# Performance work log

Hardware: AMD Instinct MI355X
Metric: run time of the kernel (lower is better)

The kernel has to match this reference:

```python
import jax, jax.numpy as jnp
import numpy as np

N_NODES = 4096
D_MODEL = 1024
MAX_DEPS = 8
N_CLASSES = 64


def setup_inputs() -> dict:
    key = jax.random.key(0)
    k1, k2, k3 = jax.random.split(key, 3)
    questions = jax.random.normal(k1, (N_NODES, D_MODEL), dtype=jnp.float32)
    # Padded dependency lists; every dependency index is strictly < node index,
    # so processing nodes in index order is a valid topological order.
    rng = np.random.default_rng(0)
    dep_idx = np.zeros((N_NODES, MAX_DEPS), dtype=np.int32)
    dep_mask = np.zeros((N_NODES, MAX_DEPS), dtype=np.int32)
    for i in range(1, N_NODES):
        nd = int(rng.integers(1, MAX_DEPS + 1))
        dep_idx[i, :nd] = rng.integers(0, i, size=nd)
        dep_mask[i, :nd] = 1
    W1 = jax.random.normal(k2, (D_MODEL, 2 * D_MODEL), dtype=jnp.float32) * 0.02
    b1 = jnp.zeros((D_MODEL,), dtype=jnp.float32)
    W2 = jax.random.normal(k3, (N_CLASSES, D_MODEL), dtype=jnp.float32) * 0.02
    b2 = jnp.zeros((N_CLASSES,), dtype=jnp.float32)
    return {
        "questions": questions,
        "W1": W1,
        "b1": b1,
        "W2": W2,
        "b2": b2,
        "dep_idx": jnp.asarray(dep_idx),
        "dep_mask": jnp.asarray(dep_mask),
    }


def reference(questions, W1, b1, W2, b2, dep_idx, dep_mask):
    n_nodes, d_model = questions.shape

    def step(answers, xs):
        i, q, deps, mask = xs
        ctx = answers[deps]                       # [MAX_DEPS, d_model] gather
        m = mask.astype(q.dtype)
        # masked mean; all-zero mask -> zero context (matches torch zeros branch)
        ctx_mean = (ctx * m[:, None]).sum(0) / jnp.maximum(m.sum(), 1.0)
        combined = jnp.concatenate([q, ctx_mean])  # [2*d_model]
        h = jax.nn.gelu(combined @ W1.T + b1, approximate=False)
        return answers.at[i].set(h), None

    answers0 = jnp.zeros((n_nodes, d_model), dtype=questions.dtype)
    xs = (jnp.arange(n_nodes), questions, dep_idx, dep_mask)
    answers, _ = jax.lax.scan(step, answers0, xs)
    root_answer = answers[n_nodes - 1]            # root = last node in topo order
    return root_answer @ W2.T + b2                # [n_classes] logits
```

## Files before the change

kernel.cpp:

```cpp
#include <hip/hip_runtime.h>

#define NN 4096
#define DM 1024
#define MD 8
#define NW 256
#define NCOL 4
#define NT 512
#define NWAVE (NT / 64)
#define UR 4
#define MAXL 4097

#define MI_NLEV 0
#define MI_ROOTPOS 1
#define MI_ARRIVE 8
#define MI_LO 1024
#define MI_NL 6144
#define MI_PERM 10240
#define MI_DCNT 14336
#define MI_INV 18432
#define MI_DPOS 22528

typedef __attribute__((ext_vector_type(8))) short bf16x8;
typedef __attribute__((ext_vector_type(8))) unsigned short ushort8;
typedef __attribute__((ext_vector_type(4))) float f32x4;

__device__ __forceinline__ float gelu_f(float x) {
  return 0.5f * x * (1.0f + erff(x * 0.70710678118654752440f));
}
__device__ __forceinline__ unsigned short f2bf(float x) {
  unsigned int u = __builtin_bit_cast(unsigned int, x);
  u += 0x7FFFu + ((u >> 16) & 1u);
  return (unsigned short)(u >> 16);
}
__device__ __forceinline__ float bf2f(unsigned short v) {
  return __builtin_bit_cast(float, (unsigned int)v << 16);
}

__global__ __launch_bounds__(1024) void k_pro(
    const float* __restrict__ Q, const int* __restrict__ dep_idx,
    const int* __restrict__ dep_mask, int* __restrict__ meta,
    unsigned short* __restrict__ Qb) {
  __shared__ unsigned short deps[NN][MD];
  __shared__ unsigned short lvl[NN];
  __shared__ unsigned short liv[NN];
  __shared__ int cnt[2 * NN];
  __shared__ int pos[NN];
  __shared__ int s_max;
  const int t = threadIdx.x;

  if (blockIdx.x != 0) {
    const size_t total = (size_t)NN * DM / 8;
    for (size_t c = (size_t)(blockIdx.x - 1) * 1024 + t; c < total; c += 256 * 1024) {
      const size_t i = c * 8;
      float4 a = *(const float4*)&Q[i];
      float4 b = *(const float4*)&Q[i + 4];
      ushort8 o;
      o[0] = f2bf(a.x); o[1] = f2bf(a.y); o[2] = f2bf(a.z); o[3] = f2bf(a.w);
      o[4] = f2bf(b.x); o[5] = f2bf(b.y); o[6] = f2bf(b.z); o[7] = f2bf(b.w);
      *(ushort8*)&Qb[i] = o;
    }
    return;
  }

  for (int i = t; i < NN; i += 1024) {
    const int4 d0 = *(const int4*)&dep_idx[i * MD];
    const int4 d1 = *(const int4*)&dep_idx[i * MD + 4];
    const int4 m0 = *(const int4*)&dep_mask[i * MD];
    const int4 m1 = *(const int4*)&dep_mask[i * MD + 4];
    deps[i][0] = m0.x ? (unsigned short)(d0.x + 1) : 0;
    deps[i][1] = m0.y ? (unsigned short)(d0.y + 1) : 0;
    deps[i][2] = m0.z ? (unsigned short)(d0.z + 1) : 0;
    deps[i][3] = m0.w ? (unsigned short)(d0.w + 1) : 0;
    deps[i][4] = m1.x ? (unsigned short)(d1.x + 1) : 0;
    deps[i][5] = m1.y ? (unsigned short)(d1.y + 1) : 0;
    deps[i][6] = m1.z ? (unsigned short)(d1.z + 1) : 0;
    deps[i][7] = m1.w ? (unsigned short)(d1.w + 1) : 0;
    lvl[i] = 0;
    liv[i] = (i == NN - 1) ? 1 : 0;
  }
  for (int i = t; i < 2 * NN; i += 1024) cnt[i] = 0;
  if (t == 0) s_max = 0;
  __syncthreads();

  if (t < 64) {
    for (int grp = 0; grp < 64; ++grp) {
      const int i = grp * 64 + t;
      const ushort8 dr = *(const ushort8*)&deps[i][0];
      int lvprev = -1;
      for (;;) {
        int m = 0;
        #pragma unroll
        for (int k = 0; k < MD; ++k) {
          const int dd = dr[k];
          if (dd) { const int l2 = (int)lvl[dd - 1] + 1; m = m > l2 ? m : l2; }
        }
        const bool ch = (m != lvprev);
        lvprev = m;
        lvl[i] = (unsigned short)m;
        if (!__any(ch)) break;
      }
    }
    for (int grp = 63; grp >= 0; --grp) {
      const int i = grp * 64 + t;
      const ushort8 dr = *(const ushort8*)&deps[i][0];
      for (;;) {
        bool ch = false;
        if (liv[i]) {
          #pragma unroll
          for (int k = 0; k < MD; ++k) {
            const int dd = dr[k];
            if (dd && !liv[dd - 1]) { liv[dd - 1] = 1; ch = true; }
          }
        }
        if (!__any(ch)) break;
      }
    }
  }
  __syncthreads();

  for (int i = t; i < NN; i += 1024) {
    const int lv = lvl[i];
    atomicAdd(&cnt[2 * lv + (liv[i] ? 0 : 1)], 1);
    atomicMax(&s_max, lv);
  }
  __syncthreads();
  const int nL = s_max + 1;
  if (t == 0) {
    int off = 0;
    for (int l = 0; l < nL; ++l) {
      meta[MI_LO + l] = off;
      meta[MI_NL + l] = cnt[2 * l];
      const int a = cnt[2 * l], b = cnt[2 * l + 1];
      cnt[2 * l] = off; off += a;
      cnt[2 * l + 1] = off; off += b;
    }
    meta[MI_LO + nL] = off;
    meta[MI_NLEV] = nL;
  }
  __syncthreads();
  for (int i = t; i < NN; i += 1024)
    pos[i] = atomicAdd(&cnt[2 * lvl[i] + (liv[i] ? 0 : 1)], 1);
  __syncthreads();
  for (int i = t; i < NN; i += 1024) {
    const int r = pos[i];
    meta[MI_PERM + r] = i;
    int nd = 0;
    #pragma unroll
    for (int k = 0; k < MD; ++k) {
      const int dd = deps[i][k];
      if (dd) { meta[MI_DPOS + r * MD + nd] = pos[dd - 1]; ++nd; }
    }
    for (int k = nd; k < MD; ++k) meta[MI_DPOS + r * MD + k] = 0;
    meta[MI_DCNT + r] = nd;
    ((float*)meta)[MI_INV + r] = nd ? 1.0f / (float)nd : 0.0f;
  }
  if (t == 0) meta[MI_ROOTPOS] = pos[NN - 1];
  for (int i = t; i < NW; i += 1024) meta[MI_ARRIVE + i] = 0;
}

__global__ __launch_bounds__(256) void k_preq(
    const unsigned short* __restrict__ Qb, const float* __restrict__ W1,
    const float* __restrict__ b1, float* __restrict__ preQ) {
  const int t = threadIdx.x;
  const int wave = t >> 6, lane = t & 63;
  const int wm = wave >> 1, wn = wave & 1;
  const int m0 = blockIdx.y * 128 + wm * 64;
  const int n0 = blockIdx.x * 128 + wn * 64;
  const int lrow = lane & 15;
  const int klo = (lane >> 4) * 8;
  f32x4 acc[4][4] = {};
  for (int k0 = 0; k0 < DM; k0 += 32) {
    bf16x8 af[4];
    #pragma unroll
    for (int f = 0; f < 4; ++f)
      af[f] = *(const bf16x8*)&Qb[(size_t)(m0 + f * 16 + lrow) * DM + k0 + klo];
    bf16x8 bfr[4];
    #pragma unroll
    for (int g = 0; g < 4; ++g) {
      const float* wsrc = &W1[(size_t)(n0 + g * 16 + lrow) * 2048 + k0 + klo];
      float4 w0 = *(const float4*)&wsrc[0];
      float4 w1 = *(const float4*)&wsrc[4];
      bf16x8 bb;
      bb[0] = (short)f2bf(w0.x); bb[1] = (short)f2bf(w0.y);
      bb[2] = (short)f2bf(w0.z); bb[3] = (short)f2bf(w0.w);
      bb[4] = (short)f2bf(w1.x); bb[5] = (short)f2bf(w1.y);
      bb[6] = (short)f2bf(w1.z); bb[7] = (short)f2bf(w1.w);
      bfr[g] = bb;
    }
    #pragma unroll
    for (int f = 0; f < 4; ++f)
      #pragma unroll
      for (int g = 0; g < 4; ++g)
        acc[f][g] = __builtin_amdgcn_mfma_f32_16x16x32_bf16(af[f], bfr[g], acc[f][g], 0, 0, 0);
  }
  float b1v[4];
  #pragma unroll
  for (int g = 0; g < 4; ++g) b1v[g] = b1[n0 + g * 16 + lrow];
  const int mrow = (lane >> 4) * 4;
  #pragma unroll
  for (int f = 0; f < 4; ++f)
    #pragma unroll
    for (int g = 0; g < 4; ++g) {
      const int n = n0 + g * 16 + lrow;
      #pragma unroll
      for (int r = 0; r < 4; ++r)
        preQ[(size_t)(m0 + f * 16 + mrow + r) * DM + n] = acc[f][g][r] + b1v[g];
    }
}

__global__ __launch_bounds__(NT) void k_levels(
    const float* __restrict__ W1, const float* __restrict__ preQ,
    unsigned short* __restrict__ hPb, float4* __restrict__ gPan, int* __restrict__ meta,
    const float* __restrict__ W2, const float* __restrict__ b2, float* __restrict__ out) {
  const int tid = threadIdx.x;
  const int wb = blockIdx.x;
  const int c0 = wb * NCOL;
  const int wave = tid >> 6, lane = tid & 63;
  const int nL = meta[MI_NLEV];
  const int rootRow = meta[MI_ROOTPOS];
  __shared__ int s_lo[MAXL];
  __shared__ int s_nl[MAXL];
  __shared__ float4 preLDS[NT];
  for (int i = tid; i <= nL; i += NT) s_lo[i] = meta[MI_LO + i];
  for (int i = tid; i < nL; i += NT) s_nl[i] = meta[MI_NL + i];
  float4 wreg[NCOL][4];
  #pragma unroll
  for (int cc = 0; cc < NCOL; ++cc)
    #pragma unroll
    for (int q = 0; q < 4; ++q)
      wreg[cc][q] = *(const float4*)&W1[(size_t)(c0 + cc) * 2048 + 1024 + lane * 16 + q * 4];
  __syncthreads();
  float4* gp = gPan + (size_t)wb * NN;
  const float* invA = (const float*)&meta[MI_INV];

  for (int l = 0; l < nL; ++l) {
    const int lo = s_lo[l];
    const int nA = s_nl[l];

    for (int r = lo + tid; r < lo + nA; r += NT) {
      const int node = meta[MI_PERM + r];
      const int nd = meta[MI_DCNT + r];
      const float iv = invA[r];
      const int4 p0 = *(const int4*)&meta[MI_DPOS + r * MD];
      const int4 p1 = *(const int4*)&meta[MI_DPOS + r * MD + 4];
      const int dps[8] = {p0.x, p0.y, p0.z, p0.w, p1.x, p1.y, p1.z, p1.w};
      float sx = 0.f, sy = 0.f, sz = 0.f, sw = 0.f;
      #pragma unroll
      for (int d = 0; d < MD; ++d) {
        float4 v = gp[dps[d]];
        sx += (d < nd) ? v.x : 0.f;
        sy += (d < nd) ? v.y : 0.f;
        sz += (d < nd) ? v.z : 0.f;
        sw += (d < nd) ? v.w : 0.f;
      }
      const float4 pq = (l > 0 && r == lo + tid) ? preLDS[tid]
                                                 : *(const float4*)&preQ[(size_t)node * DM + c0];
      const unsigned short h0 = f2bf(gelu_f(pq.x + sx * iv));
      const unsigned short h1 = f2bf(gelu_f(pq.y + sy * iv));
      const unsigned short h2 = f2bf(gelu_f(pq.z + sz * iv));
      const unsigned short h3 = f2bf(gelu_f(pq.w + sw * iv));
      const unsigned long long u = (unsigned long long)h0 | ((unsigned long long)h1 << 16)
                                 | ((unsigned long long)h2 << 32) | ((unsigned long long)h3 << 48);
      __hip_atomic_store((unsigned long long*)&hPb[(size_t)r * DM + c0], u,
                         __ATOMIC_RELAXED, __HIP_MEMORY_SCOPE_AGENT);
    }
    __syncthreads();
    if (tid == 0)
      __hip_atomic_store(&meta[MI_ARRIVE + wb], l + 1, __ATOMIC_RELAXED, __HIP_MEMORY_SCOPE_AGENT);
    if (l + 1 < nL && tid < s_nl[l + 1]) {
      const int node2 = meta[MI_PERM + s_lo[l + 1] + tid];
      preLDS[tid] = *(const float4*)&preQ[(size_t)node2 * DM + c0];
    }
    if (tid < 64) {
      for (;;) {
        int m = 1 << 30;
        #pragma unroll
        for (int u = 0; u < 4; ++u) {
          int v = __hip_atomic_load(&meta[MI_ARRIVE + tid * 4 + u], __ATOMIC_RELAXED, __HIP_MEMORY_SCOPE_AGENT);
          m = v < m ? v : m;
        }
        #pragma unroll
        for (int off = 1; off < 64; off <<= 1) {
          int o = __shfl_xor(m, off);
          m = o < m ? o : m;
        }
        if (m >= l + 1) break;
        __builtin_amdgcn_s_sleep(1);
      }
    }
    __syncthreads();

    for (int base = wave * UR; base < nA; base += NWAVE * UR) {
      const int cnt = nA - base;
      ushort8 hv[UR][2];
      #pragma unroll
      for (int u = 0; u < UR; ++u) {
        const int r = lo + base + ((u < cnt) ? u : 0);
        const ushort8* h8 = (const ushort8*)&hPb[(size_t)r * DM];
        hv[u][0] = h8[lane * 2];
        hv[u][1] = h8[lane * 2 + 1];
      }
      float rr[UR][NCOL];
      #pragma unroll
      for (int u = 0; u < UR; ++u) {
        float hf[16];
        #pragma unroll
        for (int e = 0; e < 8; ++e) { hf[e] = bf2f(hv[u][0][e]); hf[8 + e] = bf2f(hv[u][1][e]); }
        #pragma unroll
        for (int cc = 0; cc < NCOL; ++cc) {
          float a = 0.f;
          #pragma unroll
          for (int q = 0; q < 4; ++q)
            a += hf[q * 4 + 0] * wreg[cc][q].x + hf[q * 4 + 1] * wreg[cc][q].y
               + hf[q * 4 + 2] * wreg[cc][q].z + hf[q * 4 + 3] * wreg[cc][q].w;
          rr[u][cc] = a;
        }
      }
      #pragma unroll
      for (int off = 1; off < 64; off <<= 1)
        #pragma unroll
        for (int u = 0; u < UR; ++u)
          #pragma unroll
          for (int cc = 0; cc < NCOL; ++cc)
            rr[u][cc] += __shfl_xor(rr[u][cc], off);
      if (lane == 0) {
        #pragma unroll
        for (int u = 0; u < UR; ++u)
          if (u < cnt) gp[lo + base + u] = make_float4(rr[u][0], rr[u][1], rr[u][2], rr[u][3]);
      }
    }
    __syncthreads();
  }

  if (wb == 0) {
    float* red = (float*)preLDS;
    const int j = tid >> 3, kc = tid & 7;
    const ushort8* h8 = (const ushort8*)&hPb[(size_t)rootRow * DM];
    const float* wr2 = W2 + (size_t)j * DM;
    float acc = 0.f;
    for (int k = kc * 128; k < kc * 128 + 128; k += 8) {
      ushort8 hv = h8[k >> 3];
      float4 wa = *(const float4*)&wr2[k];
      float4 wb4 = *(const float4*)&wr2[k + 4];
      acc += bf2f(hv[0]) * wa.x + bf2f(hv[1]) * wa.y + bf2f(hv[2]) * wa.z + bf2f(hv[3]) * wa.w
           + bf2f(hv[4]) * wb4.x + bf2f(hv[5]) * wb4.y + bf2f(hv[6]) * wb4.z + bf2f(hv[7]) * wb4.w;
    }
    red[tid] = acc;
    __syncthreads();
    if (kc == 0) {
      float s = 0.f;
      #pragma unroll
      for (int e = 0; e < 8; ++e) s += red[j * 8 + e];
      out[j] = s + b2[j];
    }
  }
}

extern "C" void kernel_launch(void* const* d_in, const int* in_sizes, int n_in,
                              void* d_out, int out_size, void* d_ws, size_t ws_size,
                              hipStream_t stream) {
  const float* Q        = (const float*)d_in[0];
  const float* W1       = (const float*)d_in[1];
  const float* b1       = (const float*)d_in[2];
  const float* W2       = (const float*)d_in[3];
  const float* b2       = (const float*)d_in[4];
  const int*   dep_idx  = (const int*)d_in[5];
  const int*   dep_mask = (const int*)d_in[6];

  char* ws = (char*)d_ws;
  float*          preQ = (float*)ws;
  unsigned short* hPb  = (unsigned short*)(ws + (16ull << 20));
  unsigned short* Qb   = (unsigned short*)(ws + (24ull << 20));
  float4*         gPan = (float4*)(ws + (32ull << 20));
  int*            meta = (int*)(ws + (48ull << 20));
  float*          out  = (float*)d_out;

  k_pro<<<dim3(257), dim3(1024), 0, stream>>>(Q, dep_idx, dep_mask, meta, Qb);
  k_preq<<<dim3(DM / 128, NN / 128), dim3(256), 0, stream>>>(Qb, W1, b1, preQ);
  k_levels<<<dim3(NW), dim3(NT), 0, stream>>>(W1, preQ, hPb, gPan, meta, W2, b2, out);
}
```

Before: 556.4 us.

## Defer non-urgent panel products past the level barrier and parallelize level computation

Live nodes in each level are split into urgent ones, whose result is consumed by the very next level, and deferred ones. Only the urgent rows' context-panel products are computed before the per-level barrier. The deferred rows are computed during the next level, before the spin-wait, so that work overlaps the cross-block synchronization. The prologue also replaces the single-wave level and liveness propagation with a 1024-thread block-synchronous iteration, and drops one conversion block. This adds more metadata and more block barriers in the prologue.

```diff
diff --git a/kernel.cpp b/kernel.cpp
--- a/kernel.cpp
+++ b/kernel.cpp
@@ -15,10 +15,11 @@
 #define MI_ARRIVE 8
 #define MI_LO 1024
 #define MI_NL 6144
-#define MI_PERM 10240
-#define MI_DCNT 14336
-#define MI_INV 18432
-#define MI_DPOS 22528
+#define MI_NU 10240
+#define MI_PERM 14336
+#define MI_DCNT 18432
+#define MI_INV 22528
+#define MI_DPOS 26624
 
 typedef __attribute__((ext_vector_type(8))) short bf16x8;
 typedef __attribute__((ext_vector_type(8))) unsigned short ushort8;
@@ -40,17 +41,17 @@
     const float* __restrict__ Q, const int* __restrict__ dep_idx,
     const int* __restrict__ dep_mask, int* __restrict__ meta,
     unsigned short* __restrict__ Qb) {
-  __shared__ unsigned short deps[NN][MD];
-  __shared__ unsigned short lvl[NN];
-  __shared__ unsigned short liv[NN];
-  __shared__ int cnt[2 * NN];
+  __shared__ int lvl[NN];
+  __shared__ int liv[NN];
+  __shared__ int mcl[NN];
+  __shared__ int cnt[3 * NN];
   __shared__ int pos[NN];
-  __shared__ int s_max;
+  __shared__ int s_changed, s_max;
   const int t = threadIdx.x;
 
   if (blockIdx.x != 0) {
     const size_t total = (size_t)NN * DM / 8;
-    for (size_t c = (size_t)(blockIdx.x - 1) * 1024 + t; c < total; c += 256 * 1024) {
+    for (size_t c = (size_t)(blockIdx.x - 1) * 1024 + t; c < total; c += 255 * 1024) {
       const size_t i = c * 8;
       float4 a = *(const float4*)&Q[i];
       float4 b = *(const float4*)&Q[i + 4];
@@ -63,65 +64,83 @@
   }
 
   for (int i = t; i < NN; i += 1024) {
+    lvl[i] = 0; liv[i] = (i == NN - 1) ? 1 : 0; mcl[i] = 0x7FFFFFFF;
+  }
+  for (int i = t; i < 3 * NN; i += 1024) cnt[i] = 0;
+  if (t == 0) s_max = 0;
+  __syncthreads();
+
+  for (int u = 0; u < 4; ++u) {
+    const int i = u * 1024 + t;
     const int4 d0 = *(const int4*)&dep_idx[i * MD];
     const int4 d1 = *(const int4*)&dep_idx[i * MD + 4];
     const int4 m0 = *(const int4*)&dep_mask[i * MD];
     const int4 m1 = *(const int4*)&dep_mask[i * MD + 4];
-    deps[i][0] = m0.x ? (unsigned short)(d0.x + 1) : 0;
-    deps[i][1] = m0.y ? (unsigned short)(d0.y + 1) : 0;
-    deps[i][2] = m0.z ? (unsigned short)(d0.z + 1) : 0;
-    deps[i][3] = m0.w ? (unsigned short)(d0.w + 1) : 0;
-    deps[i][4] = m1.x ? (unsigned short)(d1.x + 1) : 0;
-    deps[i][5] = m1.y ? (unsigned short)(d1.y + 1) : 0;
-    deps[i][6] = m1.z ? (unsigned short)(d1.z + 1) : 0;
-    deps[i][7] = m1.w ? (unsigned short)(d1.w + 1) : 0;
-    lvl[i] = 0;
-    liv[i] = (i == NN - 1) ? 1 : 0;
-  }
-  for (int i = t; i < 2 * NN; i += 1024) cnt[i] = 0;
-  if (t == 0) s_max = 0;
-  __syncthreads();
-
-  if (t < 64) {
-    for (int grp = 0; grp < 64; ++grp) {
-      const int i = grp * 64 + t;
-      const ushort8 dr = *(const ushort8*)&deps[i][0];
-      int lvprev = -1;
-      for (;;) {
-        int m = 0;
-        #pragma unroll
-        for (int k = 0; k < MD; ++k) {
-          const int dd = dr[k];
-          if (dd) { const int l2 = (int)lvl[dd - 1] + 1; m = m > l2 ? m : l2; }
-        }
-        const bool ch = (m != lvprev);
-        lvprev = m;
-        lvl[i] = (unsigned short)m;
-        if (!__any(ch)) break;
-      }
-    }
-    for (int grp = 63; grp >= 0; --grp) {
-      const int i = grp * 64 + t;
-      const ushort8 dr = *(const ushort8*)&deps[i][0];
-      for (;;) {
-        bool ch = false;
-        if (liv[i]) {
-          #pragma unroll
-          for (int k = 0; k < MD; ++k) {
-            const int dd = dr[k];
-            if (dd && !liv[dd - 1]) { liv[dd - 1] = 1; ch = true; }
-          }
-        }
-        if (!__any(ch)) break;
-      }
-    }
-  }
-  __syncthreads();
-
+    int my = 0;
+    for (;;) {
+      if (t == 0) s_changed = 0;
+      __syncthreads();
+      int m = 0;
+      if (m0.x) { int l = lvl[d0.x] + 1; m = m > l ? m : l; }
+      if (m0.y) { int l = lvl[d0.y] + 1; m = m > l ? m : l; }
+      if (m0.z) { int l = lvl[d0.z] + 1; m = m > l ? m : l; }
+      if (m0.w) { int l = lvl[d0.w] + 1; m = m > l ? m : l; }
+      if (m1.x) { int l = lvl[d1.x] + 1; m = m > l ? m : l; }
+      if (m1.y) { int l = lvl[d1.y] + 1; m = m > l ? m : l; }
+      if (m1.z) { int l = lvl[d1.z] + 1; m = m > l ? m : l; }
+      if (m1.w) { int l = lvl[d1.w] + 1; m = m > l ? m : l; }
+      if (m > my) { my = m; lvl[i] = m; s_changed = 1; }
+      __syncthreads();
+      if (!s_changed) break;
+    }
+  }
+  for (int u = 3; u >= 0; --u) {
+    const int i = u * 1024 + t;
+    const int4 d0 = *(const int4*)&dep_idx[i * MD];
+    const int4 d1 = *(const int4*)&dep_idx[i * MD + 4];
+    const int4 m0 = *(const int4*)&dep_mask[i * MD];
+    const int4 m1 = *(const int4*)&dep_mask[i * MD + 4];
+    for (;;) {
+      if (t == 0) s_changed = 0;
+      __syncthreads();
+      bool ch = false;
+      if (liv[i]) {
+        if (m0.x && !liv[d0.x]) { liv[d0.x] = 1; ch = true; }
+        if (m0.y && !liv[d0.y]) { liv[d0.y] = 1; ch = true; }
+        if (m0.z && !liv[d0.z]) { liv[d0.z] = 1; ch = true; }
+        if (m0.w && !liv[d0.w]) { liv[d0.w] = 1; ch = true; }
+        if (m1.x && !liv[d1.x]) { liv[d1.x] = 1; ch = true; }
+        if (m1.y && !liv[d1.y]) { liv[d1.y] = 1; ch = true; }
+        if (m1.z && !liv[d1.z]) { liv[d1.z] = 1; ch = true; }
+        if (m1.w && !liv[d1.w]) { liv[d1.w] = 1; ch = true; }
+      }
+      if (ch) s_changed = 1;
+      __syncthreads();
+      if (!s_changed) break;
+    }
+  }
   for (int i = t; i < NN; i += 1024) {
-    const int lv = lvl[i];
-    atomicAdd(&cnt[2 * lv + (liv[i] ? 0 : 1)], 1);
-    atomicMax(&s_max, lv);
+    if (!liv[i]) continue;
+    const int4 d0 = *(const int4*)&dep_idx[i * MD];
+    const int4 d1 = *(const int4*)&dep_idx[i * MD + 4];
+    const int4 m0 = *(const int4*)&dep_mask[i * MD];
+    const int4 m1 = *(const int4*)&dep_mask[i * MD + 4];
+    const int L = lvl[i];
+    if (m0.x) atomicMin(&mcl[d0.x], L);
+    if (m0.y) atomicMin(&mcl[d0.y], L);
+    if (m0.z) atomicMin(&mcl[d0.z], L);
+    if (m0.w) atomicMin(&mcl[d0.w], L);
+    if (m1.x) atomicMin(&mcl[d1.x], L);
+    if (m1.y) atomicMin(&mcl[d1.y], L);
+    if (m1.z) atomicMin(&mcl[d1.z], L);
+    if (m1.w) atomicMin(&mcl[d1.w], L);
+  }
+  __syncthreads();
+  for (int i = t; i < NN; i += 1024) {
+    const int key = liv[i] ? ((mcl[i] == lvl[i] + 1) ? 0 : 1) : 2;
+    mcl[i] = key;
+    atomicAdd(&cnt[3 * lvl[i] + key], 1);
+    atomicMax(&s_max, lvl[i]);
   }
   __syncthreads();
   const int nL = s_max + 1;
@@ -129,27 +148,33 @@
     int off = 0;
     for (int l = 0; l < nL; ++l) {
       meta[MI_LO + l] = off;
-      meta[MI_NL + l] = cnt[2 * l];
-      const int a = cnt[2 * l], b = cnt[2 * l + 1];
-      cnt[2 * l] = off; off += a;
-      cnt[2 * l + 1] = off; off += b;
+      const int a = cnt[3 * l], b = cnt[3 * l + 1], c = cnt[3 * l + 2];
+      meta[MI_NU + l] = a;
+      meta[MI_NL + l] = a + b;
+      cnt[3 * l] = off; off += a;
+      cnt[3 * l + 1] = off; off += b;
+      cnt[3 * l + 2] = off; off += c;
     }
     meta[MI_LO + nL] = off;
     meta[MI_NLEV] = nL;
   }
   __syncthreads();
   for (int i = t; i < NN; i += 1024)
-    pos[i] = atomicAdd(&cnt[2 * lvl[i] + (liv[i] ? 0 : 1)], 1);
+    pos[i] = atomicAdd(&cnt[3 * lvl[i] + mcl[i]], 1);
   __syncthreads();
   for (int i = t; i < NN; i += 1024) {
     const int r = pos[i];
     meta[MI_PERM + r] = i;
+    const int4 d0 = *(const int4*)&dep_idx[i * MD];
+    const int4 d1 = *(const int4*)&dep_idx[i * MD + 4];
+    const int4 m0 = *(const int4*)&dep_mask[i * MD];
+    const int4 m1 = *(const int4*)&dep_mask[i * MD + 4];
+    const int dd[8] = {d0.x, d0.y, d0.z, d0.w, d1.x, d1.y, d1.z, d1.w};
+    const int mm[8] = {m0.x, m0.y, m0.z, m0.w, m1.x, m1.y, m1.z, m1.w};
     int nd = 0;
     #pragma unroll
-    for (int k = 0; k < MD; ++k) {
-      const int dd = deps[i][k];
-      if (dd) { meta[MI_DPOS + r * MD + nd] = pos[dd - 1]; ++nd; }
-    }
+    for (int k = 0; k < MD; ++k)
+      if (mm[k]) { meta[MI_DPOS + r * MD + nd] = pos[dd[k]]; ++nd; }
     for (int k = nd; k < MD; ++k) meta[MI_DPOS + r * MD + k] = 0;
     meta[MI_DCNT + r] = nd;
     ((float*)meta)[MI_INV + r] = nd ? 1.0f / (float)nd : 0.0f;
@@ -220,9 +245,10 @@
   const int rootRow = meta[MI_ROOTPOS];
   __shared__ int s_lo[MAXL];
   __shared__ int s_nl[MAXL];
+  __shared__ int s_nu[MAXL];
   __shared__ float4 preLDS[NT];
   for (int i = tid; i <= nL; i += NT) s_lo[i] = meta[MI_LO + i];
-  for (int i = tid; i < nL; i += NT) s_nl[i] = meta[MI_NL + i];
+  for (int i = tid; i < nL; i += NT) { s_nl[i] = meta[MI_NL + i]; s_nu[i] = meta[MI_NU + i]; }
   float4 wreg[NCOL][4];
   #pragma unroll
   for (int cc = 0; cc < NCOL; ++cc)
@@ -233,11 +259,55 @@
   float4* gp = gPan + (size_t)wb * NN;
   const float* invA = (const float*)&meta[MI_INV];
 
+  auto bphase = [&](int rlo, int rhi) {
+    for (int base = rlo + wave * UR; base < rhi; base += NWAVE * UR) {
+      const int cnt = rhi - base;
+      ushort8 hv[UR][2];
+      #pragma unroll
+      for (int u = 0; u < UR; ++u) {
+        const int r = base + ((u < cnt) ? u : 0);
+        const ushort8* h8 = (const ushort8*)&hPb[(size_t)r * DM];
+        hv[u][0] = h8[lane * 2];
+        hv[u][1] = h8[lane * 2 + 1];
+      }
+      float rr[UR][NCOL];
+      #pragma unroll
+      for (int u = 0; u < UR; ++u) {
+        float hf[16];
+        #pragma unroll
+        for (int e = 0; e < 8; ++e) { hf[e] = bf2f(hv[u][0][e]); hf[8 + e] = bf2f(hv[u][1][e]); }
+        #pragma unroll
+        for (int cc = 0; cc < NCOL; ++cc) {
+          float a = 0.f;
+          #pragma unroll
+          for (int q = 0; q < 4; ++q)
+            a += hf[q * 4 + 0] * wreg[cc][q].x + hf[q * 4 + 1] * wreg[cc][q].y
+               + hf[q * 4 + 2] * wreg[cc][q].z + hf[q * 4 + 3] * wreg[cc][q].w;
+          rr[u][cc] = a;
+        }
+      }
+      #pragma unroll
+      for (int off = 1; off < 64; off <<= 1)
+        #pragma unroll
+        for (int u = 0; u < UR; ++u)
+          #pragma unroll
+          for (int cc = 0; cc < NCOL; ++cc)
+            rr[u][cc] += __shfl_xor(rr[u][cc], off);
+      if (lane == 0) {
+        #pragma unroll
+        for (int u = 0; u < UR; ++u)
+          if (u < cnt) gp[base + u] = make_float4(rr[u][0], rr[u][1], rr[u][2], rr[u][3]);
+      }
+    }
+  };
+
+  int plo = 0, pnu = 0, pnl = 0;
   for (int l = 0; l < nL; ++l) {
     const int lo = s_lo[l];
-    const int nA = s_nl[l];
-
-    for (int r = lo + tid; r < lo + nA; r += NT) {
+    const int nl = s_nl[l];
+    const int nu = s_nu[l];
+
+    for (int r = lo + tid; r < lo + nl; r += NT) {
       const int node = meta[MI_PERM + r];
       const int nd = meta[MI_DCNT + r];
       const float iv = invA[r];
@@ -271,6 +341,7 @@
       const int node2 = meta[MI_PERM + s_lo[l + 1] + tid];
       preLDS[tid] = *(const float4*)&preQ[(size_t)node2 * DM + c0];
     }
+    bphase(plo + pnu, plo + pnl);
     if (tid < 64) {
       for (;;) {
         int m = 1 << 30;
@@ -289,46 +360,8 @@
       }
     }
     __syncthreads();
-
-    for (int base = wave * UR; base < nA; base += NWAVE * UR) {
-      const int cnt = nA - base;
-      ushort8 hv[UR][2];
-      #pragma unroll
-      for (int u = 0; u < UR; ++u) {
-        const int r = lo + base + ((u < cnt) ? u : 0);
-        const ushort8* h8 = (const ushort8*)&hPb[(size_t)r * DM];
-        hv[u][0] = h8[lane * 2];
-        hv[u][1] = h8[lane * 2 + 1];
-      }
-      float rr[UR][NCOL];
-      #pragma unroll
-      for (int u = 0; u < UR; ++u) {
-        float hf[16];
-        #pragma unroll
-        for (int e = 0; e < 8; ++e) { hf[e] = bf2f(hv[u][0][e]); hf[8 + e] = bf2f(hv[u][1][e]); }
-        #pragma unroll
-        for (int cc = 0; cc < NCOL; ++cc) {
-          float a = 0.f;
-          #pragma unroll
-          for (int q = 0; q < 4; ++q)
-            a += hf[q * 4 + 0] * wreg[cc][q].x + hf[q * 4 + 1] * wreg[cc][q].y
-               + hf[q * 4 + 2] * wreg[cc][q].z + hf[q * 4 + 3] * wreg[cc][q].w;
-          rr[u][cc] = a;
-        }
-      }
-      #pragma unroll
-      for (int off = 1; off < 64; off <<= 1)
-        #pragma unroll
-        for (int u = 0; u < UR; ++u)
-          #pragma unroll
-          for (int cc = 0; cc < NCOL; ++cc)
-            rr[u][cc] += __shfl_xor(rr[u][cc], off);
-      if (lane == 0) {
-        #pragma unroll
-        for (int u = 0; u < UR; ++u)
-          if (u < cnt) gp[lo + base + u] = make_float4(rr[u][0], rr[u][1], rr[u][2], rr[u][3]);
-      }
-    }
+    bphase(lo, lo + nu);
+    plo = lo; pnu = nu; pnl = nl;
     __syncthreads();
   }
 
@@ -375,7 +408,7 @@
   int*            meta = (int*)(ws + (48ull << 20));
   float*          out  = (float*)d_out;
 
-  k_pro<<<dim3(257), dim3(1024), 0, stream>>>(Q, dep_idx, dep_mask, meta, Qb);
+  k_pro<<<dim3(256), dim3(1024), 0, stream>>>(Q, dep_idx, dep_mask, meta, Qb);
   k_preq<<<dim3(DM / 128, NN / 128), dim3(256), 0, stream>>>(Qb, W1, b1, preQ);
   k_levels<<<dim3(NW), dim3(NT), 0, stream>>>(W1, preQ, hPb, gPan, meta, W2, b2, out);
 }
```

After: 536.0 us. 1.04x faster.
